# Optimization experiments

Measured on AMD Instinct MI355X. Metric: run time of the kernel, lower is better.

The kernel has to match this reference:

```python
import jax, jax.numpy as jnp
import numpy as np

N_USER = 100000
N_ITEM = 200000


def setup_inputs() -> dict:
    key = jax.random.key(0)
    ks = jax.random.split(key, 9)
    n = N_USER + N_ITEM
    nnz = 9600000
    return {
        "users_emb": jax.random.normal(ks[0], (N_USER, 64), dtype=jnp.float32) * 0.1,
        "items_emb": jax.random.normal(ks[1], (N_ITEM, 64), dtype=jnp.float32) * 0.1,
        "user_sim_neighbor": jax.random.randint(ks[2], (N_USER, 10), 0, N_USER),
        "user_sim_weight": jax.random.uniform(ks[3], (N_USER, 10), dtype=jnp.float32),
        "item_sim_neighbor": jax.random.randint(ks[4], (N_ITEM, 10), 0, N_ITEM),
        "item_sim_weight": jax.random.uniform(ks[5], (N_ITEM, 10), dtype=jnp.float32),
        "graph_rows": jax.random.randint(ks[6], (nnz,), 0, n),
        "graph_cols": jax.random.randint(ks[7], (nnz,), 0, n),
        "graph_vals": jax.random.uniform(ks[8], (nnz,), dtype=jnp.float32),
    }


def reference(users_emb, items_emb, user_sim_neighbor, user_sim_weight,
              item_sim_neighbor, item_sim_weight, graph_rows, graph_cols, graph_vals):
    n = users_emb.shape[0] + items_emb.shape[0]
    emb = jnp.concatenate([users_emb, items_emb], axis=0)  # [n, d]

    # top-k neighbor gather + weighted sum (users then items)
    user_neighbor_emb = jnp.einsum("nk,nkd->nd", user_sim_weight, users_emb[user_sim_neighbor])
    item_neighbor_emb = jnp.einsum("nk,nkd->nd", item_sim_weight, items_emb[item_sim_neighbor])
    neighbor_emb = jnp.concatenate([user_neighbor_emb, item_neighbor_emb], axis=0)

    # sparse graph matmul: all_emb = Graph @ emb  (COO rows/cols/vals)
    all_emb = jax.ops.segment_sum(graph_vals[:, None] * emb[graph_cols], graph_rows,
                                  num_segments=n)

    emb = emb + neighbor_emb + all_emb
    users = emb[:users_emb.shape[0]]
    items = emb[users_emb.shape[0]:]
    return users, items
```

## Files before the change

### kernel.cpp

```cpp
#include <hip/hip_runtime.h>

#define N_USER 100000
#define N_ITEM 200000
#define N_TOT  (N_USER + N_ITEM)
#define D      64
#define RPB    64
#define NB     ((N_TOT + RPB - 1) / RPB)
#define NSB    ((NB + 63) / 64)
#define SLICES 8
#define NBLK_A 512
#define NBLK_C 256
#define CAP    2304
#define SCAN_CHUNK 2048

__device__ __forceinline__ unsigned short f2bf(float f) {
    unsigned b = __float_as_uint(f);
    unsigned r = (b + 0x7FFFu + ((b >> 16) & 1u)) >> 16;
    return (unsigned short)r;
}
__device__ __forceinline__ float bf2f(unsigned short u) {
    return __uint_as_float(((unsigned)u) << 16);
}

__global__ __launch_bounds__(256) void conv_kernel(const float* __restrict__ users,
                                                   const float* __restrict__ items,
                                                   ushort* __restrict__ emb16) {
    size_t i = (size_t)blockIdx.x * blockDim.x + threadIdx.x;
    const size_t total = (size_t)N_TOT * D / 4;
    if (i >= total) return;
    size_t e0 = i * 4;
    const size_t usz = (size_t)N_USER * D;
    const float* src = (e0 < usz) ? users + e0 : items + (e0 - usz);
    float4 v = *reinterpret_cast<const float4*>(src);
    ushort4 o;
    o.x = f2bf(v.x); o.y = f2bf(v.y); o.z = f2bf(v.z); o.w = f2bf(v.w);
    *reinterpret_cast<ushort4*>(emb16 + e0) = o;
}

__global__ __launch_bounds__(512) void count2_kernel(const int* __restrict__ rows,
                                                     int* __restrict__ totB, int nnz, int chunk) {
    __shared__ int h[NB];
    for (int k = threadIdx.x; k < NB; k += 512) h[k] = 0;
    __syncthreads();
    int lo = blockIdx.x * chunk;
    int hi = min(lo + chunk, nnz);
    for (int i = lo + threadIdx.x; i < hi; i += 512)
        atomicAdd(&h[rows[i] >> 6], 1);
    __syncthreads();
    for (int k = threadIdx.x; k < NB; k += 512)
        if (h[k]) atomicAdd(&totB[k], h[k]);
}

__global__ __launch_bounds__(1024) void scan_kernel(const int* __restrict__ totB,
                                                    int* __restrict__ bstart,
                                                    int* __restrict__ gcurB,
                                                    int* __restrict__ gcurA, int nnz) {
    __shared__ int s[1024];
    const int t = threadIdx.x;
    const int PER = (NB + 1023) / 1024;
    int loc[8];
    int sum = 0;
    #pragma unroll
    for (int k = 0; k < PER; ++k) {
        int idx = t * PER + k;
        int v = (idx < NB) ? totB[idx] : 0;
        loc[k] = sum; sum += v;
    }
    s[t] = sum;
    __syncthreads();
    for (int off = 1; off < 1024; off <<= 1) {
        int v = (t >= off) ? s[t - off] : 0;
        __syncthreads();
        s[t] += v;
        __syncthreads();
    }
    int base = s[t] - sum;
    #pragma unroll
    for (int k = 0; k < PER; ++k) {
        int idx = t * PER + k;
        if (idx < NB) { bstart[idx] = base + loc[k]; gcurB[idx] = base + loc[k]; }
    }
    if (t == 1023) bstart[NB] = nnz;
    __syncthreads();
    if (t < NSB) gcurA[t] = bstart[t * 64];
}

__global__ __launch_bounds__(512) void binA_kernel(const int* __restrict__ rows,
                                                   const int* __restrict__ cols,
                                                   const float* __restrict__ vals,
                                                   int* __restrict__ gcurA,
                                                   uint2* __restrict__ eg1, int nnz, int chunk) {
    __shared__ int h[NSB];
    if (threadIdx.x < NSB) h[threadIdx.x] = 0;
    __syncthreads();
    int lo = blockIdx.x * chunk;
    int hi = min(lo + chunk, nnz);
    for (int i = lo + threadIdx.x; i < hi; i += 512)
        atomicAdd(&h[rows[i] >> 12], 1);
    __syncthreads();
    if (threadIdx.x < NSB && h[threadIdx.x])
        h[threadIdx.x] = atomicAdd(&gcurA[threadIdx.x], h[threadIdx.x]);
    __syncthreads();
    for (int i = lo + threadIdx.x; i < hi; i += 512) {
        int r = rows[i];
        int slot = atomicAdd(&h[r >> 12], 1);
        uint2 p;
        p.x = ((unsigned)(r & 4095) << 19) | (unsigned)cols[i];
        p.y = __float_as_uint(vals[i]);
        eg1[slot] = p;
    }
}

__global__ __launch_bounds__(512) void binB_kernel(const int* __restrict__ bstart,
                                                   int* __restrict__ gcurB,
                                                   const uint2* __restrict__ eg1,
                                                   uint2* __restrict__ eg2) {
    __shared__ int h[64];
    const int sb    = blockIdx.x / SLICES;
    const int slice = blockIdx.x % SLICES;
    const int s0 = bstart[sb * 64];
    const int e0 = bstart[min((sb + 1) * 64, NB)];
    const int len = e0 - s0;
    const int chunk = (len + SLICES - 1) / SLICES;
    const int lo = s0 + slice * chunk;
    const int hi = min(lo + chunk, e0);

    if (threadIdx.x < 64) h[threadIdx.x] = 0;
    __syncthreads();
    for (int i = lo + threadIdx.x; i < hi; i += 512)
        atomicAdd(&h[(eg1[i].x >> 25) & 63], 1);
    __syncthreads();
    if (threadIdx.x < 64 && h[threadIdx.x])
        h[threadIdx.x] = atomicAdd(&gcurB[sb * 64 + threadIdx.x], h[threadIdx.x]);
    __syncthreads();
    for (int i = lo + threadIdx.x; i < hi; i += 512) {
        uint2 p = eg1[i];
        int slot = atomicAdd(&h[(p.x >> 25) & 63], 1);
        eg2[slot] = p;
    }
}

__global__ __launch_bounds__(256) void sortgather_kernel(
    const ushort* __restrict__ emb16,
    const int*   __restrict__ unb,   const float* __restrict__ uw,
    const int*   __restrict__ inb,   const float* __restrict__ iw,
    const int*   __restrict__ bstart, const uint2* __restrict__ eg,
    float* __restrict__ out)
{
    __shared__ uint2 lds_e[CAP];
    __shared__ int h[RPB], st[RPB], cur[RPB];

    const int tid  = threadIdx.x;
    const int g    = tid >> 4;
    const int sub  = tid & 15;
    const int d0   = sub * 4;
    const int k    = blockIdx.x;
    const int row0 = k * RPB;

    float4 acc[4];
    #pragma unroll
    for (int rr = 0; rr < 4; ++rr) {
        const int row = row0 + rr * 16 + g;
        if (row >= N_TOT) { acc[rr] = make_float4(0.f, 0.f, 0.f, 0.f); continue; }
        ushort4 ub = *reinterpret_cast<const ushort4*>(emb16 + (size_t)row * D + d0);
        float4 a = make_float4(bf2f(ub.x), bf2f(ub.y), bf2f(ub.z), bf2f(ub.w));
        if (row < N_USER) {
            const int*   nb = unb + (size_t)row * 10;
            const float* w  = uw  + (size_t)row * 10;
            #pragma unroll
            for (int q = 0; q < 10; ++q) {
                ushort4 u = *reinterpret_cast<const ushort4*>(emb16 + (size_t)nb[q] * D + d0);
                float wq = w[q];
                a.x += wq * bf2f(u.x); a.y += wq * bf2f(u.y);
                a.z += wq * bf2f(u.z); a.w += wq * bf2f(u.w);
            }
        } else {
            const int r = row - N_USER;
            const int*   nb = inb + (size_t)r * 10;
            const float* w  = iw  + (size_t)r * 10;
            #pragma unroll
            for (int q = 0; q < 10; ++q) {
                ushort4 u = *reinterpret_cast<const ushort4*>(emb16 + ((size_t)nb[q] + N_USER) * D + d0);
                float wq = w[q];
                a.x += wq * bf2f(u.x); a.y += wq * bf2f(u.y);
                a.z += wq * bf2f(u.z); a.w += wq * bf2f(u.w);
            }
        }
        acc[rr] = a;
    }

    const int s = bstart[k];
    const int e = bstart[k + 1];

    for (int cs = s; cs < e; cs += CAP) {
        const int n = min(e - cs, CAP);

        if (tid < RPB) h[tid] = 0;
        __syncthreads();
        for (int i = tid; i < n; i += 256)
            atomicAdd(&h[(eg[cs + i].x >> 19) & 63], 1);
        __syncthreads();
        if (tid < RPB) {
            int orig = h[tid];
            int v = orig;
            #pragma unroll
            for (int off = 1; off < RPB; off <<= 1) {
                int u = __shfl_up(v, off);
                if (tid >= off) v += u;
            }
            st[tid]  = v - orig;
            cur[tid] = v - orig;
        }
        __syncthreads();
        for (int i = tid; i < n; i += 256) {
            uint2 p = eg[cs + i];
            int slot = atomicAdd(&cur[(p.x >> 19) & 63], 1);
            lds_e[slot] = p;
        }
        __syncthreads();

        #pragma unroll
        for (int rr = 0; rr < 4; ++rr) {
            const int r  = rr * 16 + g;
            const int b0 = st[r];
            const int cr = h[r];
            int j = 0;
            for (; j + 3 < cr; j += 4) {
                uint2 p0 = lds_e[b0 + j],     p1 = lds_e[b0 + j + 1];
                uint2 p2 = lds_e[b0 + j + 2], p3 = lds_e[b0 + j + 3];
                ushort4 u0 = *reinterpret_cast<const ushort4*>(emb16 + (size_t)(p0.x & 0x7FFFFu) * D + d0);
                ushort4 u1 = *reinterpret_cast<const ushort4*>(emb16 + (size_t)(p1.x & 0x7FFFFu) * D + d0);
                ushort4 u2 = *reinterpret_cast<const ushort4*>(emb16 + (size_t)(p2.x & 0x7FFFFu) * D + d0);
                ushort4 u3 = *reinterpret_cast<const ushort4*>(emb16 + (size_t)(p3.x & 0x7FFFFu) * D + d0);
                float a0 = __uint_as_float(p0.y), a1 = __uint_as_float(p1.y);
                float a2 = __uint_as_float(p2.y), a3 = __uint_as_float(p3.y);
                acc[rr].x += a0 * bf2f(u0.x); acc[rr].y += a0 * bf2f(u0.y);
                acc[rr].z += a0 * bf2f(u0.z); acc[rr].w += a0 * bf2f(u0.w);
                acc[rr].x += a1 * bf2f(u1.x); acc[rr].y += a1 * bf2f(u1.y);
                acc[rr].z += a1 * bf2f(u1.z); acc[rr].w += a1 * bf2f(u1.w);
                acc[rr].x += a2 * bf2f(u2.x); acc[rr].y += a2 * bf2f(u2.y);
                acc[rr].z += a2 * bf2f(u2.z); acc[rr].w += a2 * bf2f(u2.w);
                acc[rr].x += a3 * bf2f(u3.x); acc[rr].y += a3 * bf2f(u3.y);
                acc[rr].z += a3 * bf2f(u3.z); acc[rr].w += a3 * bf2f(u3.w);
            }
            for (; j < cr; ++j) {
                uint2 p = lds_e[b0 + j];
                ushort4 u = *reinterpret_cast<const ushort4*>(emb16 + (size_t)(p.x & 0x7FFFFu) * D + d0);
                float a = __uint_as_float(p.y);
                acc[rr].x += a * bf2f(u.x); acc[rr].y += a * bf2f(u.y);
                acc[rr].z += a * bf2f(u.z); acc[rr].w += a * bf2f(u.w);
            }
        }
        __syncthreads();
    }

    #pragma unroll
    for (int rr = 0; rr < 4; ++rr) {
        const int row = row0 + rr * 16 + g;
        if (row < N_TOT)
            *reinterpret_cast<float4*>(&out[(size_t)row * D + d0]) = acc[rr];
    }
}


__global__ void count_kernel(const int* __restrict__ rows, int* __restrict__ cnt, int nnz) {
    int i = blockIdx.x * blockDim.x + threadIdx.x;
    int stride = gridDim.x * blockDim.x;
    for (; i < nnz; i += stride) atomicAdd(&cnt[rows[i]], 1);
}

__global__ void scan_block_sums(const int* __restrict__ cnt, int* __restrict__ bsum, int n) {
    __shared__ int sdata[256];
    int base = blockIdx.x * SCAN_CHUNK;
    int s = 0;
    for (int t = threadIdx.x; t < SCAN_CHUNK; t += 256) {
        int idx = base + t;
        s += (idx < n) ? cnt[idx] : 0;
    }
    sdata[threadIdx.x] = s;
    __syncthreads();
    for (int off = 128; off > 0; off >>= 1) {
        if (threadIdx.x < off) sdata[threadIdx.x] += sdata[threadIdx.x + off];
        __syncthreads();
    }
    if (threadIdx.x == 0) bsum[blockIdx.x] = sdata[0];
}

__global__ void scan_bsum_kernel(int* __restrict__ bsum, int nb) {
    if (threadIdx.x == 0 && blockIdx.x == 0) {
        int acc = 0;
        for (int i = 0; i < nb; ++i) { int v = bsum[i]; bsum[i] = acc; acc += v; }
    }
}

__global__ void scan_final(const int* __restrict__ cnt, const int* __restrict__ bsum,
                           int* __restrict__ row_start, int n, int nnz) {
    __shared__ int sums[256];
    int b = blockIdx.x, t = threadIdx.x;
    int base = b * SCAN_CHUNK;
    int loc[8];
    int s = 0;
    #pragma unroll
    for (int k = 0; k < 8; ++k) {
        int idx = base + t * 8 + k;
        int v = (idx < n) ? cnt[idx] : 0;
        loc[k] = s; s += v;
    }
    sums[t] = s;
    __syncthreads();
    for (int off = 1; off < 256; off <<= 1) {
        int v = (t >= off) ? sums[t - off] : 0;
        __syncthreads();
        sums[t] += v;
        __syncthreads();
    }
    int off0 = bsum[b] + (sums[t] - s);
    #pragma unroll
    for (int k = 0; k < 8; ++k) {
        int idx = base + t * 8 + k;
        if (idx < n) row_start[idx] = off0 + loc[k];
    }
    if (b == gridDim.x - 1 && t == 255) row_start[n] = nnz;
}

__global__ void fill_kernel(const int* __restrict__ rows, const int* __restrict__ cols,
                            const float* __restrict__ vals, const int* __restrict__ row_start,
                            int* __restrict__ pos, uint2* __restrict__ eg, int nnz) {
    int i = blockIdx.x * blockDim.x + threadIdx.x;
    int stride = gridDim.x * blockDim.x;
    for (; i < nnz; i += stride) {
        int r = rows[i];
        int p = atomicAdd(&pos[r], 1);
        uint2 e;
        e.x = (unsigned)cols[i];
        e.y = __float_as_uint(vals[i]);
        eg[row_start[r] + p] = e;
    }
}

__global__ __launch_bounds__(256) void gather16_kernel(
    const float* __restrict__ users, const float* __restrict__ items,
    const int*   __restrict__ unb,   const float* __restrict__ uw,
    const int*   __restrict__ inb,   const float* __restrict__ iw,
    const int*   __restrict__ row_start, const uint2* __restrict__ eg,
    float* __restrict__ out)
{
    const int tid = threadIdx.x;
    const int grp = tid >> 4;
    const int sub = tid & 15;
    const int row = blockIdx.x * 16 + grp;
    if (row >= N_TOT) return;
    const int d0 = sub * 4;

    float4 acc;
    if (row < N_USER) {
        acc = *reinterpret_cast<const float4*>(&users[(size_t)row * D + d0]);
        const int*   nb = unb + (size_t)row * 10;
        const float* w  = uw  + (size_t)row * 10;
        #pragma unroll
        for (int q = 0; q < 10; ++q) {
            float4 v = *reinterpret_cast<const float4*>(&users[(size_t)nb[q] * D + d0]);
            float wq = w[q];
            acc.x += wq * v.x; acc.y += wq * v.y; acc.z += wq * v.z; acc.w += wq * v.w;
        }
    } else {
        int r = row - N_USER;
        acc = *reinterpret_cast<const float4*>(&items[(size_t)r * D + d0]);
        const int*   nb = inb + (size_t)r * 10;
        const float* w  = iw  + (size_t)r * 10;
        #pragma unroll
        for (int q = 0; q < 10; ++q) {
            float4 v = *reinterpret_cast<const float4*>(&items[(size_t)nb[q] * D + d0]);
            float wq = w[q];
            acc.x += wq * v.x; acc.y += wq * v.y; acc.z += wq * v.z; acc.w += wq * v.w;
        }
    }

    const int s = row_start[row];
    const int e = row_start[row + 1];
    for (int i = s; i < e; ++i) {
        uint2 p = eg[i];
        int c = (int)(p.x & 0x7FFFFu);
        const float* src = (c < N_USER) ? users + (size_t)c * D : items + (size_t)(c - N_USER) * D;
        float4 v = *reinterpret_cast<const float4*>(src + d0);
        float a = __uint_as_float(p.y);
        acc.x += a * v.x; acc.y += a * v.y; acc.z += a * v.z; acc.w += a * v.w;
    }

    *reinterpret_cast<float4*>(&out[(size_t)row * D + d0]) = acc;
}

__global__ __launch_bounds__(256) void base_neighbor_kernel(
    const float* __restrict__ users, const float* __restrict__ items,
    const int*   __restrict__ unb,   const float* __restrict__ uw,
    const int*   __restrict__ inb,   const float* __restrict__ iw,
    float* __restrict__ out)
{
    int gtid = blockIdx.x * blockDim.x + threadIdx.x;
    int row  = gtid >> 6;
    int lane = gtid & 63;
    if (row >= N_TOT) return;
    float acc;
    if (row < N_USER) {
        acc = users[(size_t)row * D + lane];
        const int*   nb = unb + (size_t)row * 10;
        const float* w  = uw  + (size_t)row * 10;
        #pragma unroll
        for (int q = 0; q < 10; ++q) acc += w[q] * users[(size_t)nb[q] * D + lane];
    } else {
        int r = row - N_USER;
        acc = items[(size_t)r * D + lane];
        const int*   nb = inb + (size_t)r * 10;
        const float* w  = iw  + (size_t)r * 10;
        #pragma unroll
        for (int q = 0; q < 10; ++q) acc += w[q] * items[(size_t)nb[q] * D + lane];
    }
    out[(size_t)row * D + lane] = acc;
}

__global__ __launch_bounds__(256) void edge_scatter_kernel(
    const float* __restrict__ users, const float* __restrict__ items,
    const int*   __restrict__ rows,  const int* __restrict__ cols,
    const float* __restrict__ vals,
    float* __restrict__ out, int nnz)
{
    int gtid = blockIdx.x * blockDim.x + threadIdx.x;
    int e    = gtid >> 6;
    int lane = gtid & 63;
    if (e >= nnz) return;
    int   r = rows[e];
    int   c = cols[e];
    float v = vals[e];
    const float* src = (c < N_USER) ? (users + (size_t)c * D)
                                    : (items + (size_t)(c - N_USER) * D);
    atomicAdd(&out[(size_t)r * D + lane], v * src[lane]);
}

extern "C" void kernel_launch(void* const* d_in, const int* in_sizes, int n_in,
                              void* d_out, int out_size, void* d_ws, size_t ws_size,
                              hipStream_t stream) {
    const float* users = (const float*)d_in[0];
    const float* items = (const float*)d_in[1];
    const int*   unb   = (const int*)  d_in[2];
    const float* uw    = (const float*)d_in[3];
    const int*   inb   = (const int*)  d_in[4];
    const float* iw    = (const float*)d_in[5];
    const int*   grow  = (const int*)  d_in[6];
    const int*   gcol  = (const int*)  d_in[7];
    const float* gval  = (const float*)d_in[8];
    float* out = (float*)d_out;

    const int nnz = in_sizes[6];

    const size_t A = 255;
    const size_t sz_eg       = (((size_t)nnz * 8) + A) & ~A;
    const size_t sz_bstart   = (((size_t)(NB + 1) * 4) + A) & ~A;
    const size_t sz_gcurB    = (((size_t)NB * 4) + A) & ~A;
    const size_t sz_gcurA    = (((size_t)NSB * 4) + A) & ~A;
    const size_t sz_totB     = (((size_t)NB * 4) + A) & ~A;
    const size_t sz_emb16    = (((size_t)N_TOT * D * 2) + A) & ~A;
    const size_t sz_rowstart = (((size_t)(N_TOT + 1) * 4) + A) & ~A;
    const size_t need0 = 2 * sz_eg + sz_bstart + sz_gcurB + sz_gcurA + sz_totB + sz_emb16;

    const size_t sz_cnt  = (((size_t)N_TOT * 4) + A) & ~A;
    const int    nb2     = (N_TOT + SCAN_CHUNK - 1) / SCAN_CHUNK;
    const size_t sz_bsum = (((size_t)nb2 * 4) + A) & ~A;
    const size_t need2 = sz_eg + sz_rowstart + sz_cnt + sz_bsum;

    if (ws_size >= need0) {
        char* wsp = (char*)d_ws;
        uint2*  eg1    = (uint2*)wsp;  wsp += sz_eg;
        uint2*  eg2    = (uint2*)wsp;  wsp += sz_eg;
        int*    bstart = (int*)wsp;    wsp += sz_bstart;
        int*    gcurB  = (int*)wsp;    wsp += sz_gcurB;
        int*    gcurA  = (int*)wsp;    wsp += sz_gcurA;
        int*    totB   = (int*)wsp;    wsp += sz_totB;
        ushort* emb16  = (ushort*)wsp;

        const int chunkC = (nnz + NBLK_C - 1) / NBLK_C;
        const int chunkA = (nnz + NBLK_A - 1) / NBLK_A;
        const int conv_grid = (int)(((size_t)N_TOT * D / 4 + 255) / 256);

        conv_kernel<<<conv_grid, 256, 0, stream>>>(users, items, emb16);
        hipMemsetAsync(totB, 0, (size_t)NB * 4, stream);
        count2_kernel<<<NBLK_C, 512, 0, stream>>>(grow, totB, nnz, chunkC);
        scan_kernel<<<1, 1024, 0, stream>>>(totB, bstart, gcurB, gcurA, nnz);
        binA_kernel<<<NBLK_A, 512, 0, stream>>>(grow, gcol, gval, gcurA, eg1, nnz, chunkA);
        binB_kernel<<<NSB * SLICES, 512, 0, stream>>>(bstart, gcurB, eg1, eg2);
        sortgather_kernel<<<NB, 256, 0, stream>>>(emb16, unb, uw, inb, iw,
                                                  bstart, eg2, out);
    } else if (ws_size >= need2) {
        char* wsp = (char*)d_ws;
        uint2* eg        = (uint2*)wsp;  wsp += sz_eg;
        int*   row_start = (int*)wsp;    wsp += sz_rowstart;
        int*   cnt       = (int*)wsp;    wsp += sz_cnt;
        int*   bsum      = (int*)wsp;

        hipMemsetAsync(cnt, 0, (size_t)N_TOT * 4, stream);
        count_kernel<<<2048, 256, 0, stream>>>(grow, cnt, nnz);
        scan_block_sums<<<nb2, 256, 0, stream>>>(cnt, bsum, N_TOT);
        scan_bsum_kernel<<<1, 64, 0, stream>>>(bsum, nb2);
        scan_final<<<nb2, 256, 0, stream>>>(cnt, bsum, row_start, N_TOT, nnz);
        hipMemsetAsync(cnt, 0, (size_t)N_TOT * 4, stream);
        fill_kernel<<<2048, 256, 0, stream>>>(grow, gcol, gval, row_start, cnt, eg, nnz);
        const int g16_grid = (N_TOT + 15) / 16;
        gather16_kernel<<<g16_grid, 256, 0, stream>>>(users, items, unb, uw, inb, iw,
                                                      row_start, eg, out);
    } else {
        int grid = (int)(((long long)N_TOT * 64 + 255) / 256);
        base_neighbor_kernel<<<grid, 256, 0, stream>>>(users, items, unb, uw, inb, iw, out);
        long long ethreads = (long long)nnz * 64;
        long long egrid = (ethreads + 255) / 256;
        edge_scatter_kernel<<<(int)egrid, 256, 0, stream>>>(users, items, grow, gcol, gval, out, nnz);
    }
}
```

Baseline: 487.3 us.

## Drop global row count pass, use fixed-capacity superbins and bf16 edge values

```diff
diff --git a/kernel.cpp b/kernel.cpp
--- a/kernel.cpp
+++ b/kernel.cpp
@@ -9,8 +9,7 @@
 #define NSB    ((NB + 63) / 64)
 #define SLICES 8
 #define NBLK_A 512
-#define NBLK_C 256
-#define CAP    2304
+#define CAP    2560
 #define SCAN_CHUNK 2048
 
 __device__ __forceinline__ unsigned short f2bf(float f) {
@@ -37,106 +36,107 @@
     *reinterpret_cast<ushort4*>(emb16 + e0) = o;
 }
 
-__global__ __launch_bounds__(512) void count2_kernel(const int* __restrict__ rows,
-                                                     int* __restrict__ totB, int nnz, int chunk) {
-    __shared__ int h[NB];
-    for (int k = threadIdx.x; k < NB; k += 512) h[k] = 0;
-    __syncthreads();
-    int lo = blockIdx.x * chunk;
-    int hi = min(lo + chunk, nnz);
-    for (int i = lo + threadIdx.x; i < hi; i += 512)
-        atomicAdd(&h[rows[i] >> 6], 1);
-    __syncthreads();
-    for (int k = threadIdx.x; k < NB; k += 512)
-        if (h[k]) atomicAdd(&totB[k], h[k]);
-}
-
-__global__ __launch_bounds__(1024) void scan_kernel(const int* __restrict__ totB,
-                                                    int* __restrict__ bstart,
-                                                    int* __restrict__ gcurB,
-                                                    int* __restrict__ gcurA, int nnz) {
-    __shared__ int s[1024];
-    const int t = threadIdx.x;
-    const int PER = (NB + 1023) / 1024;
-    int loc[8];
-    int sum = 0;
-    #pragma unroll
-    for (int k = 0; k < PER; ++k) {
-        int idx = t * PER + k;
-        int v = (idx < NB) ? totB[idx] : 0;
-        loc[k] = sum; sum += v;
-    }
-    s[t] = sum;
-    __syncthreads();
-    for (int off = 1; off < 1024; off <<= 1) {
-        int v = (t >= off) ? s[t - off] : 0;
-        __syncthreads();
-        s[t] += v;
-        __syncthreads();
-    }
-    int base = s[t] - sum;
-    #pragma unroll
-    for (int k = 0; k < PER; ++k) {
-        int idx = t * PER + k;
-        if (idx < NB) { bstart[idx] = base + loc[k]; gcurB[idx] = base + loc[k]; }
-    }
-    if (t == 1023) bstart[NB] = nnz;
-    __syncthreads();
-    if (t < NSB) gcurA[t] = bstart[t * 64];
-}
-
 __global__ __launch_bounds__(512) void binA_kernel(const int* __restrict__ rows,
                                                    const int* __restrict__ cols,
                                                    const float* __restrict__ vals,
                                                    int* __restrict__ gcurA,
-                                                   uint2* __restrict__ eg1, int nnz, int chunk) {
+                                                   unsigned* __restrict__ eg1m,
+                                                   ushort* __restrict__ eg1v,
+                                                   int nnz, int chunk, int cap_s) {
     __shared__ int h[NSB];
-    if (threadIdx.x < NSB) h[threadIdx.x] = 0;
+    const int tid = threadIdx.x;
+    if (tid < NSB) h[tid] = 0;
     __syncthreads();
     int lo = blockIdx.x * chunk;
     int hi = min(lo + chunk, nnz);
+    for (int i = lo + tid; i < hi; i += 512)
+        atomicAdd(&h[rows[i] >> 12], 1);
+    __syncthreads();
+    if (tid < NSB && h[tid])
+        h[tid] = atomicAdd(&gcurA[tid], h[tid]);
+    __syncthreads();
+    for (int i = lo + tid; i < hi; i += 512) {
+        int r = rows[i];
+        int s = r >> 12;
+        int slot = atomicAdd(&h[s], 1);
+        size_t p = (size_t)s * cap_s + slot;
+        eg1m[p] = ((unsigned)(r & 4095) << 19) | (unsigned)cols[i];
+        eg1v[p] = f2bf(vals[i]);
+    }
+}
+
+__global__ __launch_bounds__(512) void binBh_kernel(const int* __restrict__ lenA,
+                                                    const unsigned* __restrict__ eg1m,
+                                                    int* __restrict__ H, int cap_s) {
+    __shared__ int h[64];
+    const int sb = blockIdx.x / SLICES;
+    const int sl = blockIdx.x % SLICES;
+    const int len = lenA[sb];
+    const int chunk = (len + SLICES - 1) / SLICES;
+    const int lo = sl * chunk;
+    const int hi = min(lo + chunk, len);
+    const size_t base = (size_t)sb * cap_s;
+    if (threadIdx.x < 64) h[threadIdx.x] = 0;
+    __syncthreads();
     for (int i = lo + threadIdx.x; i < hi; i += 512)
-        atomicAdd(&h[rows[i] >> 12], 1);
-    __syncthreads();
-    if (threadIdx.x < NSB && h[threadIdx.x])
-        h[threadIdx.x] = atomicAdd(&gcurA[threadIdx.x], h[threadIdx.x]);
+        atomicAdd(&h[(eg1m[base + i] >> 25) & 63], 1);
+    __syncthreads();
+    if (threadIdx.x < 64)
+        H[((size_t)sb * SLICES + sl) * 64 + threadIdx.x] = h[threadIdx.x];
+}
+
+__global__ __launch_bounds__(128) void scan_all(const int* __restrict__ lenA,
+                                                int* __restrict__ H,
+                                                int* __restrict__ bstart, int nnz) {
+    __shared__ int ss[NSB + 1];
+    const int t = threadIdx.x;
+    if (t == 0) {
+        int acc = 0;
+        for (int s = 0; s < NSB; ++s) { ss[s] = acc; acc += lenA[s]; }
+        ss[NSB] = acc;
+    }
+    __syncthreads();
+    for (int sb = t; sb < NSB; sb += 128) {
+        int base = ss[sb];
+        int nbk = min(64, NB - sb * 64);
+        for (int b = 0; b < nbk; ++b) {
+            bstart[sb * 64 + b] = base;
+            int cur = base;
+            for (int sl = 0; sl < SLICES; ++sl) {
+                size_t idx = ((size_t)sb * SLICES + sl) * 64 + b;
+                int c = H[idx];
+                H[idx] = cur;
+                cur += c;
+            }
+            base = cur;
+        }
+    }
+    if (t == 0) bstart[NB] = nnz;
+}
+
+__global__ __launch_bounds__(512) void binBs_kernel(const int* __restrict__ lenA,
+                                                    const unsigned* __restrict__ eg1m,
+                                                    const ushort* __restrict__ eg1v,
+                                                    const int* __restrict__ H,
+                                                    unsigned* __restrict__ eg2m,
+                                                    ushort* __restrict__ eg2v, int cap_s) {
+    __shared__ int cur[64];
+    const int sb = blockIdx.x / SLICES;
+    const int sl = blockIdx.x % SLICES;
+    const int len = lenA[sb];
+    const int chunk = (len + SLICES - 1) / SLICES;
+    const int lo = sl * chunk;
+    const int hi = min(lo + chunk, len);
+    const size_t base = (size_t)sb * cap_s;
+    if (threadIdx.x < 64)
+        cur[threadIdx.x] = H[((size_t)sb * SLICES + sl) * 64 + threadIdx.x];
     __syncthreads();
     for (int i = lo + threadIdx.x; i < hi; i += 512) {
-        int r = rows[i];
-        int slot = atomicAdd(&h[r >> 12], 1);
-        uint2 p;
-        p.x = ((unsigned)(r & 4095) << 19) | (unsigned)cols[i];
-        p.y = __float_as_uint(vals[i]);
-        eg1[slot] = p;
-    }
-}
-
-__global__ __launch_bounds__(512) void binB_kernel(const int* __restrict__ bstart,
-                                                   int* __restrict__ gcurB,
-                                                   const uint2* __restrict__ eg1,
-                                                   uint2* __restrict__ eg2) {
-    __shared__ int h[64];
-    const int sb    = blockIdx.x / SLICES;
-    const int slice = blockIdx.x % SLICES;
-    const int s0 = bstart[sb * 64];
-    const int e0 = bstart[min((sb + 1) * 64, NB)];
-    const int len = e0 - s0;
-    const int chunk = (len + SLICES - 1) / SLICES;
-    const int lo = s0 + slice * chunk;
-    const int hi = min(lo + chunk, e0);
-
-    if (threadIdx.x < 64) h[threadIdx.x] = 0;
-    __syncthreads();
-    for (int i = lo + threadIdx.x; i < hi; i += 512)
-        atomicAdd(&h[(eg1[i].x >> 25) & 63], 1);
-    __syncthreads();
-    if (threadIdx.x < 64 && h[threadIdx.x])
-        h[threadIdx.x] = atomicAdd(&gcurB[sb * 64 + threadIdx.x], h[threadIdx.x]);
-    __syncthreads();
-    for (int i = lo + threadIdx.x; i < hi; i += 512) {
-        uint2 p = eg1[i];
-        int slot = atomicAdd(&h[(p.x >> 25) & 63], 1);
-        eg2[slot] = p;
+        unsigned m = eg1m[base + i];
+        ushort  v = eg1v[base + i];
+        int slot = atomicAdd(&cur[(m >> 25) & 63], 1);
+        eg2m[slot] = m;
+        eg2v[slot] = v;
     }
 }
 
@@ -144,10 +144,12 @@
     const ushort* __restrict__ emb16,
     const int*   __restrict__ unb,   const float* __restrict__ uw,
     const int*   __restrict__ inb,   const float* __restrict__ iw,
-    const int*   __restrict__ bstart, const uint2* __restrict__ eg,
+    const int*   __restrict__ bstart,
+    const unsigned* __restrict__ eg2m, const ushort* __restrict__ eg2v,
     float* __restrict__ out)
 {
-    __shared__ uint2 lds_e[CAP];
+    __shared__ unsigned lds_m[CAP];
+    __shared__ ushort   lds_v[CAP];
     __shared__ int h[RPB], st[RPB], cur[RPB];
 
     const int tid  = threadIdx.x;
@@ -198,7 +200,7 @@
         if (tid < RPB) h[tid] = 0;
         __syncthreads();
         for (int i = tid; i < n; i += 256)
-            atomicAdd(&h[(eg[cs + i].x >> 19) & 63], 1);
+            atomicAdd(&h[(eg2m[cs + i] >> 19) & 63], 1);
         __syncthreads();
         if (tid < RPB) {
             int orig = h[tid];
@@ -213,9 +215,11 @@
         }
         __syncthreads();
         for (int i = tid; i < n; i += 256) {
-            uint2 p = eg[cs + i];
-            int slot = atomicAdd(&cur[(p.x >> 19) & 63], 1);
-            lds_e[slot] = p;
+            unsigned m = eg2m[cs + i];
+            ushort  v = eg2v[cs + i];
+            int slot = atomicAdd(&cur[(m >> 19) & 63], 1);
+            lds_m[slot] = m;
+            lds_v[slot] = v;
         }
         __syncthreads();
 
@@ -226,14 +230,14 @@
             const int cr = h[r];
             int j = 0;
             for (; j + 3 < cr; j += 4) {
-                uint2 p0 = lds_e[b0 + j],     p1 = lds_e[b0 + j + 1];
-                uint2 p2 = lds_e[b0 + j + 2], p3 = lds_e[b0 + j + 3];
-                ushort4 u0 = *reinterpret_cast<const ushort4*>(emb16 + (size_t)(p0.x & 0x7FFFFu) * D + d0);
-                ushort4 u1 = *reinterpret_cast<const ushort4*>(emb16 + (size_t)(p1.x & 0x7FFFFu) * D + d0);
-                ushort4 u2 = *reinterpret_cast<const ushort4*>(emb16 + (size_t)(p2.x & 0x7FFFFu) * D + d0);
-                ushort4 u3 = *reinterpret_cast<const ushort4*>(emb16 + (size_t)(p3.x & 0x7FFFFu) * D + d0);
-                float a0 = __uint_as_float(p0.y), a1 = __uint_as_float(p1.y);
-                float a2 = __uint_as_float(p2.y), a3 = __uint_as_float(p3.y);
+                unsigned m0 = lds_m[b0 + j],     m1 = lds_m[b0 + j + 1];
+                unsigned m2 = lds_m[b0 + j + 2], m3 = lds_m[b0 + j + 3];
+                float a0 = bf2f(lds_v[b0 + j]),     a1 = bf2f(lds_v[b0 + j + 1]);
+                float a2 = bf2f(lds_v[b0 + j + 2]), a3 = bf2f(lds_v[b0 + j + 3]);
+                ushort4 u0 = *reinterpret_cast<const ushort4*>(emb16 + (size_t)(m0 & 0x7FFFFu) * D + d0);
+                ushort4 u1 = *reinterpret_cast<const ushort4*>(emb16 + (size_t)(m1 & 0x7FFFFu) * D + d0);
+                ushort4 u2 = *reinterpret_cast<const ushort4*>(emb16 + (size_t)(m2 & 0x7FFFFu) * D + d0);
+                ushort4 u3 = *reinterpret_cast<const ushort4*>(emb16 + (size_t)(m3 & 0x7FFFFu) * D + d0);
                 acc[rr].x += a0 * bf2f(u0.x); acc[rr].y += a0 * bf2f(u0.y);
                 acc[rr].z += a0 * bf2f(u0.z); acc[rr].w += a0 * bf2f(u0.w);
                 acc[rr].x += a1 * bf2f(u1.x); acc[rr].y += a1 * bf2f(u1.y);
@@ -244,9 +248,9 @@
                 acc[rr].z += a3 * bf2f(u3.z); acc[rr].w += a3 * bf2f(u3.w);
             }
             for (; j < cr; ++j) {
-                uint2 p = lds_e[b0 + j];
-                ushort4 u = *reinterpret_cast<const ushort4*>(emb16 + (size_t)(p.x & 0x7FFFFu) * D + d0);
-                float a = __uint_as_float(p.y);
+                unsigned m = lds_m[b0 + j];
+                float a = bf2f(lds_v[b0 + j]);
+                ushort4 u = *reinterpret_cast<const ushort4*>(emb16 + (size_t)(m & 0x7FFFFu) * D + d0);
                 acc[rr].x += a * bf2f(u.x); acc[rr].y += a * bf2f(u.y);
                 acc[rr].z += a * bf2f(u.z); acc[rr].w += a * bf2f(u.w);
             }
@@ -451,17 +455,22 @@
     float* out = (float*)d_out;
 
     const int nnz = in_sizes[6];
+    const int cap_s = nnz / NSB + 16384;
 
     const size_t A = 255;
+    const size_t sz_eg1m   = (((size_t)NSB * cap_s * 4) + A) & ~A;
+    const size_t sz_eg1v   = (((size_t)NSB * cap_s * 2) + A) & ~A;
+    const size_t sz_eg2m   = (((size_t)nnz * 4) + A) & ~A;
+    const size_t sz_eg2v   = (((size_t)nnz * 2) + A) & ~A;
+    const size_t sz_H      = (((size_t)NSB * SLICES * 64 * 4) + A) & ~A;
+    const size_t sz_bstart = (((size_t)(NB + 1) * 4) + A) & ~A;
+    const size_t sz_gcurA  = (((size_t)NSB * 4) + A) & ~A;
+    const size_t sz_emb16  = (((size_t)N_TOT * D * 2) + A) & ~A;
+    const size_t need0 = sz_eg1m + sz_eg1v + sz_eg2m + sz_eg2v + sz_H
+                       + sz_bstart + sz_gcurA + sz_emb16;
+
     const size_t sz_eg       = (((size_t)nnz * 8) + A) & ~A;
-    const size_t sz_bstart   = (((size_t)(NB + 1) * 4) + A) & ~A;
-    const size_t sz_gcurB    = (((size_t)NB * 4) + A) & ~A;
-    const size_t sz_gcurA    = (((size_t)NSB * 4) + A) & ~A;
-    const size_t sz_totB     = (((size_t)NB * 4) + A) & ~A;
-    const size_t sz_emb16    = (((size_t)N_TOT * D * 2) + A) & ~A;
     const size_t sz_rowstart = (((size_t)(N_TOT + 1) * 4) + A) & ~A;
-    const size_t need0 = 2 * sz_eg + sz_bstart + sz_gcurB + sz_gcurA + sz_totB + sz_emb16;
-
     const size_t sz_cnt  = (((size_t)N_TOT * 4) + A) & ~A;
     const int    nb2     = (N_TOT + SCAN_CHUNK - 1) / SCAN_CHUNK;
     const size_t sz_bsum = (((size_t)nb2 * 4) + A) & ~A;
@@ -469,26 +478,28 @@
 
     if (ws_size >= need0) {
         char* wsp = (char*)d_ws;
-        uint2*  eg1    = (uint2*)wsp;  wsp += sz_eg;
-        uint2*  eg2    = (uint2*)wsp;  wsp += sz_eg;
-        int*    bstart = (int*)wsp;    wsp += sz_bstart;
-        int*    gcurB  = (int*)wsp;    wsp += sz_gcurB;
-        int*    gcurA  = (int*)wsp;    wsp += sz_gcurA;
-        int*    totB   = (int*)wsp;    wsp += sz_totB;
-        ushort* emb16  = (ushort*)wsp;
-
-        const int chunkC = (nnz + NBLK_C - 1) / NBLK_C;
+        unsigned* eg1m   = (unsigned*)wsp;  wsp += sz_eg1m;
+        ushort*   eg1v   = (ushort*)wsp;    wsp += sz_eg1v;
+        unsigned* eg2m   = (unsigned*)wsp;  wsp += sz_eg2m;
+        ushort*   eg2v   = (ushort*)wsp;    wsp += sz_eg2v;
+        int*      H      = (int*)wsp;       wsp += sz_H;
+        int*      bstart = (int*)wsp;       wsp += sz_bstart;
+        int*      gcurA  = (int*)wsp;       wsp += sz_gcurA;
+        ushort*   emb16  = (ushort*)wsp;
+
         const int chunkA = (nnz + NBLK_A - 1) / NBLK_A;
         const int conv_grid = (int)(((size_t)N_TOT * D / 4 + 255) / 256);
 
         conv_kernel<<<conv_grid, 256, 0, stream>>>(users, items, emb16);
-        hipMemsetAsync(totB, 0, (size_t)NB * 4, stream);
-        count2_kernel<<<NBLK_C, 512, 0, stream>>>(grow, totB, nnz, chunkC);
-        scan_kernel<<<1, 1024, 0, stream>>>(totB, bstart, gcurB, gcurA, nnz);
-        binA_kernel<<<NBLK_A, 512, 0, stream>>>(grow, gcol, gval, gcurA, eg1, nnz, chunkA);
-        binB_kernel<<<NSB * SLICES, 512, 0, stream>>>(bstart, gcurB, eg1, eg2);
+        hipMemsetAsync(gcurA, 0, (size_t)NSB * 4, stream);
+        binA_kernel<<<NBLK_A, 512, 0, stream>>>(grow, gcol, gval, gcurA,
+                                                eg1m, eg1v, nnz, chunkA, cap_s);
+        binBh_kernel<<<NSB * SLICES, 512, 0, stream>>>(gcurA, eg1m, H, cap_s);
+        scan_all<<<1, 128, 0, stream>>>(gcurA, H, bstart, nnz);
+        binBs_kernel<<<NSB * SLICES, 512, 0, stream>>>(gcurA, eg1m, eg1v, H,
+                                                       eg2m, eg2v, cap_s);
         sortgather_kernel<<<NB, 256, 0, stream>>>(emb16, unb, uw, inb, iw,
-                                                  bstart, eg2, out);
+                                                  bstart, eg2m, eg2v, out);
     } else if (ws_size >= need2) {
         char* wsp = (char*)d_ws;
         uint2* eg        = (uint2*)wsp;  wsp += sz_eg;
```

Measured after the change: 570.4 us. 1.17x slower.

## Fuse row counting into coarse binning pass with fixed-capacity superbin buckets

Applied to the files above, without the earlier changes.

```diff
diff --git a/kernel.cpp b/kernel.cpp
--- a/kernel.cpp
+++ b/kernel.cpp
@@ -7,9 +7,9 @@
 #define RPB    64
 #define NB     ((N_TOT + RPB - 1) / RPB)
 #define NSB    ((NB + 63) / 64)
+#define NBH    (NSB * 64)
 #define SLICES 8
 #define NBLK_A 512
-#define NBLK_C 256
 #define CAP    2304
 #define SCAN_CHUNK 2048
 
@@ -37,24 +37,58 @@
     *reinterpret_cast<ushort4*>(emb16 + e0) = o;
 }
 
-__global__ __launch_bounds__(512) void count2_kernel(const int* __restrict__ rows,
-                                                     int* __restrict__ totB, int nnz, int chunk) {
-    __shared__ int h[NB];
-    for (int k = threadIdx.x; k < NB; k += 512) h[k] = 0;
-    __syncthreads();
-    int lo = blockIdx.x * chunk;
-    int hi = min(lo + chunk, nnz);
-    for (int i = lo + threadIdx.x; i < hi; i += 512)
+__global__ __launch_bounds__(512) void binA_kernel(const int* __restrict__ rows,
+                                                   const int* __restrict__ cols,
+                                                   const float* __restrict__ vals,
+                                                   int* __restrict__ totB,
+                                                   int* __restrict__ gcurA,
+                                                   uint2* __restrict__ eg1,
+                                                   int nnz, int chunk, int cap_s) {
+    __shared__ int h[NBH];
+    __shared__ int sp[NSB * 4];
+    __shared__ int sbase[NSB];
+    const int tid = threadIdx.x;
+
+    for (int k = tid; k < NBH; k += 512) h[k] = 0;
+    __syncthreads();
+
+    const int lo = blockIdx.x * chunk;
+    const int hi = min(lo + chunk, nnz);
+    for (int i = lo + tid; i < hi; i += 512)
         atomicAdd(&h[rows[i] >> 6], 1);
     __syncthreads();
-    for (int k = threadIdx.x; k < NB; k += 512)
+
+    for (int k = tid; k < NB; k += 512)
         if (h[k]) atomicAdd(&totB[k], h[k]);
+
+    if (tid < NSB * 4) {
+        const int s = tid >> 2, part = tid & 3;
+        int acc = 0;
+        #pragma unroll
+        for (int j = 0; j < 16; ++j) acc += h[s * 64 + part * 16 + j];
+        sp[tid] = acc;
+    }
+    __syncthreads();
+    if (tid < NSB) {
+        int tot = sp[tid * 4] + sp[tid * 4 + 1] + sp[tid * 4 + 2] + sp[tid * 4 + 3];
+        sbase[tid] = tot ? atomicAdd(&gcurA[tid], tot) : 0;
+    }
+    __syncthreads();
+
+    for (int i = lo + tid; i < hi; i += 512) {
+        int r = rows[i];
+        int s = r >> 12;
+        int slot = atomicAdd(&sbase[s], 1);
+        uint2 p;
+        p.x = ((unsigned)(r & 4095) << 19) | (unsigned)cols[i];
+        p.y = __float_as_uint(vals[i]);
+        eg1[(size_t)s * cap_s + slot] = p;
+    }
 }
 
 __global__ __launch_bounds__(1024) void scan_kernel(const int* __restrict__ totB,
                                                     int* __restrict__ bstart,
-                                                    int* __restrict__ gcurB,
-                                                    int* __restrict__ gcurA, int nnz) {
+                                                    int* __restrict__ gcurB, int nnz) {
     __shared__ int s[1024];
     const int t = threadIdx.x;
     const int PER = (NB + 1023) / 1024;
@@ -81,60 +115,34 @@
         if (idx < NB) { bstart[idx] = base + loc[k]; gcurB[idx] = base + loc[k]; }
     }
     if (t == 1023) bstart[NB] = nnz;
-    __syncthreads();
-    if (t < NSB) gcurA[t] = bstart[t * 64];
-}
-
-__global__ __launch_bounds__(512) void binA_kernel(const int* __restrict__ rows,
-                                                   const int* __restrict__ cols,
-                                                   const float* __restrict__ vals,
-                                                   int* __restrict__ gcurA,
-                                                   uint2* __restrict__ eg1, int nnz, int chunk) {
-    __shared__ int h[NSB];
-    if (threadIdx.x < NSB) h[threadIdx.x] = 0;
-    __syncthreads();
-    int lo = blockIdx.x * chunk;
-    int hi = min(lo + chunk, nnz);
-    for (int i = lo + threadIdx.x; i < hi; i += 512)
-        atomicAdd(&h[rows[i] >> 12], 1);
-    __syncthreads();
-    if (threadIdx.x < NSB && h[threadIdx.x])
-        h[threadIdx.x] = atomicAdd(&gcurA[threadIdx.x], h[threadIdx.x]);
-    __syncthreads();
-    for (int i = lo + threadIdx.x; i < hi; i += 512) {
-        int r = rows[i];
-        int slot = atomicAdd(&h[r >> 12], 1);
-        uint2 p;
-        p.x = ((unsigned)(r & 4095) << 19) | (unsigned)cols[i];
-        p.y = __float_as_uint(vals[i]);
-        eg1[slot] = p;
-    }
-}
-
-__global__ __launch_bounds__(512) void binB_kernel(const int* __restrict__ bstart,
+}
+
+__global__ __launch_bounds__(512) void binB_kernel(const int* __restrict__ lenA,
                                                    int* __restrict__ gcurB,
                                                    const uint2* __restrict__ eg1,
-                                                   uint2* __restrict__ eg2) {
+                                                   uint2* __restrict__ eg2, int cap_s) {
     __shared__ int h[64];
-    const int sb    = blockIdx.x / SLICES;
-    const int slice = blockIdx.x % SLICES;
-    const int s0 = bstart[sb * 64];
-    const int e0 = bstart[min((sb + 1) * 64, NB)];
-    const int len = e0 - s0;
+    const int sb = blockIdx.x / SLICES;
+    const int sl = blockIdx.x % SLICES;
+    const int len = lenA[sb];
     const int chunk = (len + SLICES - 1) / SLICES;
-    const int lo = s0 + slice * chunk;
-    const int hi = min(lo + chunk, e0);
+    const int lo = sl * chunk;
+    const int hi = min(lo + chunk, len);
+    const size_t base = (size_t)sb * cap_s;
 
     if (threadIdx.x < 64) h[threadIdx.x] = 0;
     __syncthreads();
     for (int i = lo + threadIdx.x; i < hi; i += 512)
-        atomicAdd(&h[(eg1[i].x >> 25) & 63], 1);
-    __syncthreads();
-    if (threadIdx.x < 64 && h[threadIdx.x])
-        h[threadIdx.x] = atomicAdd(&gcurB[sb * 64 + threadIdx.x], h[threadIdx.x]);
+        atomicAdd(&h[(eg1[base + i].x >> 25) & 63], 1);
+    __syncthreads();
+    if (threadIdx.x < 64) {
+        int b = sb * 64 + threadIdx.x;
+        if (b < NB && h[threadIdx.x])
+            h[threadIdx.x] = atomicAdd(&gcurB[b], h[threadIdx.x]);
+    }
     __syncthreads();
     for (int i = lo + threadIdx.x; i < hi; i += 512) {
-        uint2 p = eg1[i];
+        uint2 p = eg1[base + i];
         int slot = atomicAdd(&h[(p.x >> 25) & 63], 1);
         eg2[slot] = p;
     }
@@ -451,17 +459,20 @@
     float* out = (float*)d_out;
 
     const int nnz = in_sizes[6];
+    const int cap_s = nnz / NSB + 16384;
 
     const size_t A = 255;
+    const size_t sz_eg1    = (((size_t)NSB * cap_s * 8) + A) & ~A;
+    const size_t sz_eg2    = (((size_t)nnz * 8) + A) & ~A;
+    const size_t sz_totB   = (((size_t)NB * 4) + A) & ~A;
+    const size_t sz_bstart = (((size_t)(NB + 1) * 4) + A) & ~A;
+    const size_t sz_gcurB  = (((size_t)NB * 4) + A) & ~A;
+    const size_t sz_gcurA  = (((size_t)NSB * 4) + A) & ~A;
+    const size_t sz_emb16  = (((size_t)N_TOT * D * 2) + A) & ~A;
+    const size_t need0 = sz_eg1 + sz_eg2 + sz_totB + sz_bstart + sz_gcurB + sz_gcurA + sz_emb16;
+
     const size_t sz_eg       = (((size_t)nnz * 8) + A) & ~A;
-    const size_t sz_bstart   = (((size_t)(NB + 1) * 4) + A) & ~A;
-    const size_t sz_gcurB    = (((size_t)NB * 4) + A) & ~A;
-    const size_t sz_gcurA    = (((size_t)NSB * 4) + A) & ~A;
-    const size_t sz_totB     = (((size_t)NB * 4) + A) & ~A;
-    const size_t sz_emb16    = (((size_t)N_TOT * D * 2) + A) & ~A;
     const size_t sz_rowstart = (((size_t)(N_TOT + 1) * 4) + A) & ~A;
-    const size_t need0 = 2 * sz_eg + sz_bstart + sz_gcurB + sz_gcurA + sz_totB + sz_emb16;
-
     const size_t sz_cnt  = (((size_t)N_TOT * 4) + A) & ~A;
     const int    nb2     = (N_TOT + SCAN_CHUNK - 1) / SCAN_CHUNK;
     const size_t sz_bsum = (((size_t)nb2 * 4) + A) & ~A;
@@ -469,24 +480,24 @@
 
     if (ws_size >= need0) {
         char* wsp = (char*)d_ws;
-        uint2*  eg1    = (uint2*)wsp;  wsp += sz_eg;
-        uint2*  eg2    = (uint2*)wsp;  wsp += sz_eg;
+        uint2*  eg1    = (uint2*)wsp;  wsp += sz_eg1;
+        uint2*  eg2    = (uint2*)wsp;  wsp += sz_eg2;
+        int*    totB   = (int*)wsp;    wsp += sz_totB;
         int*    bstart = (int*)wsp;    wsp += sz_bstart;
         int*    gcurB  = (int*)wsp;    wsp += sz_gcurB;
         int*    gcurA  = (int*)wsp;    wsp += sz_gcurA;
-        int*    totB   = (int*)wsp;    wsp += sz_totB;
         ushort* emb16  = (ushort*)wsp;
 
-        const int chunkC = (nnz + NBLK_C - 1) / NBLK_C;
         const int chunkA = (nnz + NBLK_A - 1) / NBLK_A;
         const int conv_grid = (int)(((size_t)N_TOT * D / 4 + 255) / 256);
 
         conv_kernel<<<conv_grid, 256, 0, stream>>>(users, items, emb16);
         hipMemsetAsync(totB, 0, (size_t)NB * 4, stream);
-        count2_kernel<<<NBLK_C, 512, 0, stream>>>(grow, totB, nnz, chunkC);
-        scan_kernel<<<1, 1024, 0, stream>>>(totB, bstart, gcurB, gcurA, nnz);
-        binA_kernel<<<NBLK_A, 512, 0, stream>>>(grow, gcol, gval, gcurA, eg1, nnz, chunkA);
-        binB_kernel<<<NSB * SLICES, 512, 0, stream>>>(bstart, gcurB, eg1, eg2);
+        hipMemsetAsync(gcurA, 0, (size_t)NSB * 4, stream);
+        binA_kernel<<<NBLK_A, 512, 0, stream>>>(grow, gcol, gval, totB, gcurA,
+                                                eg1, nnz, chunkA, cap_s);
+        scan_kernel<<<1, 1024, 0, stream>>>(totB, bstart, gcurB, nnz);
+        binB_kernel<<<NSB * SLICES, 512, 0, stream>>>(gcurA, gcurB, eg1, eg2, cap_s);
         sortgather_kernel<<<NB, 256, 0, stream>>>(emb16, unb, uw, inb, iw,
                                                   bstart, eg2, out);
     } else if (ws_size >= need2) {
```

Result: faster. 465.2 us (-4.5%).
